# Optimization experiments

Measured on AMD Instinct MI355X. Metric: run time of the kernel, lower is better.

The kernel has to match this reference:

```python
import jax, jax.numpy as jnp
import numpy as np

EPS = 1e-10


def setup_inputs() -> dict:
    key = jax.random.key(0)
    k1, k2, k3 = jax.random.split(key, 3)
    B, N, S = 2, 16384, 4096
    return {
        "xyz": jax.random.normal(k1, (B, 3, N), dtype=jnp.float32),
        "sparse_xyz": jax.random.normal(k2, (B, 3, S), dtype=jnp.float32),
        "sparse_flow": jax.random.normal(k3, (B, 3, S), dtype=jnp.float32),
    }


def reference(xyz, sparse_xyz, sparse_flow):
    # channel-last views: x [B,N,3], s [B,S,3], f [B,S,3]
    x = jnp.transpose(xyz, (0, 2, 1))
    s = jnp.transpose(sparse_xyz, (0, 2, 1))
    f = jnp.transpose(sparse_flow, (0, 2, 1))

    # squared pairwise distances [B,N,S] (knn_point / square_distance)
    d2 = (
        jnp.sum(x * x, axis=-1)[:, :, None]
        + jnp.sum(s * s, axis=-1)[:, None, :]
        - 2.0 * jnp.einsum("bnc,bsc->bns", x, s)
    )
    # 3 nearest sparse neighbors of each dense point
    _, knn_idx = jax.lax.top_k(-d2, 3)  # [B,N,3]

    # index_points_group: gather neighbor coords/flows per batch
    gather = jax.vmap(lambda tbl, idx: tbl[idx])  # ([S,3],[N,3]) -> [N,3,3]
    grouped_xyz = gather(s, knn_idx)              # [B,N,3,3]
    grouped_flow = gather(f, knn_idx)             # [B,N,3,3]

    # inverse-distance weights (Euclidean dist, clamped)
    diff = grouped_xyz - x[:, :, None, :]
    dist = jnp.maximum(jnp.linalg.norm(diff, axis=3), EPS)  # [B,N,3]
    inv = 1.0 / dist
    weight = inv / jnp.sum(inv, axis=2, keepdims=True)      # [B,N,3]

    dense_flow = jnp.sum(weight[..., None] * grouped_flow, axis=2)  # [B,N,3]
    return jnp.transpose(dense_flow, (0, 2, 1))  # [B,3,N]
```

## Files before the change

### kernel.cpp

```cpp
#include <hip/hip_runtime.h>


constexpr int S_SPARSE = 4096;
constexpr int NSPLIT   = 64;
constexpr int Q        = 8;
constexpr int THREADS  = 256;
constexpr int PPB      = THREADS * Q / NSPLIT;
constexpr int NITER    = S_SPARSE / NSPLIT;
constexpr int K        = 3;
constexpr int KA       = 5;
constexpr int KM       = 8;
constexpr int KROW     = NSPLIT * K + 8;
constexpr int KBUF2_OFF_DW = PPB * KROW;
constexpr int SLIN_PAD = 64;

__device__ __forceinline__ unsigned med3u(unsigned a, unsigned b, unsigned c) {
    unsigned d;
    asm("v_med3_u32 %0, %1, %2, %3" : "=v"(d) : "v"(a), "v"(b), "v"(c));
    return d;
}

__global__ __launch_bounds__(THREADS)
void upsample_knn3(const float* __restrict__ xyz,
                   const float* __restrict__ sxyz,
                   const float* __restrict__ sflow,
                   float* __restrict__ out,
                   int N)
{
    __shared__ __align__(16) unsigned char smem_raw[(3 * S_SPARSE + SLIN_PAD) * 4];
    float*    slin = reinterpret_cast<float*>(smem_raw);
    unsigned* kbuf = reinterpret_cast<unsigned*>(smem_raw);

    const int b = blockIdx.y;
    const int t = threadIdx.x;
    const int g = t >> 6;
    const int s = t & 63;

    const float* sx = sxyz + (size_t)b * 3 * S_SPARSE;
    const float* sy = sx + S_SPARSE;
    const float* sz = sy + S_SPARSE;
    #pragma unroll
    for (int it = 0; it < 3 * S_SPARSE / (THREADS * 4); ++it) {
        const int j0 = (t + it * THREADS) * 4;
        *reinterpret_cast<float4*>(slin + j0) =
            *reinterpret_cast<const float4*>(sx + j0);
    }

    const float* xb = xyz + (size_t)b * 3 * N;
    const int p0 = blockIdx.x * PPB + g * Q;
    float qx[Q], qy[Q], qz[Q];
    {
        const float4 x0 = *reinterpret_cast<const float4*>(xb + p0);
        const float4 x1 = *reinterpret_cast<const float4*>(xb + p0 + 4);
        const float4 y0 = *reinterpret_cast<const float4*>(xb + N + p0);
        const float4 y1 = *reinterpret_cast<const float4*>(xb + N + p0 + 4);
        const float4 z0 = *reinterpret_cast<const float4*>(xb + 2 * N + p0);
        const float4 z1 = *reinterpret_cast<const float4*>(xb + 2 * N + p0 + 4);
        qx[0]=x0.x; qx[1]=x0.y; qx[2]=x0.z; qx[3]=x0.w; qx[4]=x1.x; qx[5]=x1.y; qx[6]=x1.z; qx[7]=x1.w;
        qy[0]=y0.x; qy[1]=y0.y; qy[2]=y0.z; qy[3]=y0.w; qy[4]=y1.x; qy[5]=y1.y; qy[6]=y1.z; qy[7]=y1.w;
        qz[0]=z0.x; qz[1]=z0.y; qz[2]=z0.z; qz[3]=z0.w; qz[4]=z1.x; qz[5]=z1.y; qz[6]=z1.z; qz[7]=z1.w;
    }
    __syncthreads();

    unsigned k0[Q], k1[Q], k2[Q];
    #pragma unroll
    for (int q = 0; q < Q; ++q) { k0[q]=0xFFFFFFFFu; k1[q]=0xFFFFFFFFu; k2[q]=0xFFFFFFFFu; }

    float px = slin[s], py = slin[s + S_SPARSE], pz = slin[s + 2 * S_SPARSE];

    #pragma unroll 4
    for (int i = 0; i < NITER; ++i) {
        const float cx = px, cy = py, cz = pz;
        const int   cj = (i << 6) | s;
        const int   jn = cj + 64;
        px = slin[jn];
        py = slin[jn + S_SPARSE];
        pz = slin[jn + 2 * S_SPARSE];
        #pragma unroll
        for (int q = 0; q < Q; ++q) {
            const float dx = qx[q] - cx;
            const float dy = qy[q] - cy;
            const float dz = qz[q] - cz;
            const float d2 = dx * dx + dy * dy + dz * dz;
            const unsigned c = (__float_as_uint(d2) & 0xFFFFF000u) | (unsigned)cj;
            k2[q] = med3u(k1[q], k2[q], c);
            k1[q] = med3u(k0[q], k1[q], c);
            k0[q] = min(k0[q], c);
        }
    }

    __syncthreads();
    #pragma unroll
    for (int q = 0; q < Q; ++q) {
        const int base = (g * Q + q) * KROW + s * K;
        kbuf[base + 0] = k0[q];
        kbuf[base + 1] = k1[q];
        kbuf[base + 2] = k2[q];
    }
    __syncthreads();

    {
        const int lp = t >> 3;
        const int ch = t & 7;
        unsigned m0=0xFFFFFFFFu, m1=0xFFFFFFFFu, m2=0xFFFFFFFFu, m3=0xFFFFFFFFu, m4=0xFFFFFFFFu;
        const unsigned* rowp = kbuf + lp * KROW + ch * 24;
        #pragma unroll
        for (int c = 0; c < 24; ++c) {
            const unsigned cc = rowp[c];
            m4 = med3u(m3, m4, cc);
            m3 = med3u(m2, m3, cc);
            m2 = med3u(m1, m2, cc);
            m1 = med3u(m0, m1, cc);
            m0 = min(m0, cc);
        }
        unsigned* o = kbuf + KBUF2_OFF_DW + (lp * 8 + ch) * KA;
        o[0]=m0; o[1]=m1; o[2]=m2; o[3]=m3; o[4]=m4;
    }
    __syncthreads();

    if (t < PPB) {
        unsigned bk[KM];
        #pragma unroll
        for (int k = 0; k < KM; ++k) bk[k] = 0xFFFFFFFFu;
        const unsigned* inp = kbuf + KBUF2_OFF_DW + t * 8 * KA;
        #pragma unroll
        for (int c = 0; c < 8 * KA; ++c) {
            const unsigned cc = inp[c];
            bk[7] = med3u(bk[6], bk[7], cc);
            bk[6] = med3u(bk[5], bk[6], cc);
            bk[5] = med3u(bk[4], bk[5], cc);
            bk[4] = med3u(bk[3], bk[4], cc);
            bk[3] = med3u(bk[2], bk[3], cc);
            bk[2] = med3u(bk[1], bk[2], cc);
            bk[1] = med3u(bk[0], bk[1], cc);
            bk[0] = min(bk[0], cc);
        }

        const int pt = blockIdx.x * PPB + t;
        const double qxd = (double)xb[pt];
        const double qyd = (double)xb[N + pt];
        const double qzd = (double)xb[2 * N + pt];

        double e0 = 1e300, e1 = 1e300, e2 = 1e300;
        int    j0 = 0,     j1 = 0,     j2 = 0;
        #pragma unroll
        for (int c = 0; c < KM; ++c) {
            const int    j  = (int)(bk[c] & 0xFFFu);
            const double dx = qxd - (double)sx[j];
            const double dy = qyd - (double)sy[j];
            const double dz = qzd - (double)sz[j];
            const double d2 = dx * dx + dy * dy + dz * dz;
            if (d2 < e2) {
                if (d2 < e1) {
                    e2 = e1; j2 = j1;
                    if (d2 < e0) { e1 = e0; j1 = j0; e0 = d2; j0 = j; }
                    else         { e1 = d2; j1 = j; }
                } else {
                    e2 = d2; j2 = j;
                }
            }
        }

        double dist0 = sqrt(e0); dist0 = dist0 > 1e-10 ? dist0 : 1e-10;
        double dist1 = sqrt(e1); dist1 = dist1 > 1e-10 ? dist1 : 1e-10;
        double dist2 = sqrt(e2); dist2 = dist2 > 1e-10 ? dist2 : 1e-10;
        const double inv0 = 1.0 / dist0;
        const double inv1 = 1.0 / dist1;
        const double inv2 = 1.0 / dist2;
        const double wsum = inv0 + inv1 + inv2;

        const float* fb = sflow + (size_t)b * 3 * S_SPARSE;
        float*       ob = out   + (size_t)b * 3 * N;
        #pragma unroll
        for (int c = 0; c < 3; ++c) {
            const float* fc = fb + c * S_SPARSE;
            const double o =
                (inv0 * (double)fc[j0] +
                 inv1 * (double)fc[j1] +
                 inv2 * (double)fc[j2]) / wsum;
            ob[c * N + pt] = (float)o;
        }
    }
}

extern "C" void kernel_launch(void* const* d_in, const int* in_sizes, int n_in,
                              void* d_out, int out_size, void* d_ws, size_t ws_size,
                              hipStream_t stream)
{
    const float* xyz  = (const float*)d_in[0];
    const float* sxyz = (const float*)d_in[1];
    const float* sflw = (const float*)d_in[2];
    float*       out  = (float*)d_out;

    const int B = 2;
    const int N = in_sizes[0] / (3 * B);

    dim3 grid(N / PPB, B);
    upsample_knn3<<<grid, THREADS, 0, stream>>>(xyz, sxyz, sflw, out, N);
}
```

Baseline: 44.22 us.

## Use expanded dot-product distance with packed float4 sparse points and 512-thread blocks

Sparse points are repacked in shared memory as float4 (x,y,z,|p|^2), so the inner loop issues one LDS per candidate and computes distance as three FMAs plus an add. A small positive offset keeps the value non-negative so the unsigned-key trick still works. The block grows to 512 threads and 64 points with a min-blocks hint, changing occupancy. The expanded form loses precision through cancellation, but the double-precision rescoring of the top-8 candidates should absorb this.

```diff
diff --git a/kernel.cpp b/kernel.cpp
--- a/kernel.cpp
+++ b/kernel.cpp
@@ -4,15 +4,15 @@
 constexpr int S_SPARSE = 4096;
 constexpr int NSPLIT   = 64;
 constexpr int Q        = 8;
-constexpr int THREADS  = 256;
-constexpr int PPB      = THREADS * Q / NSPLIT;
+constexpr int THREADS  = 512;
+constexpr int PPB      = 64;
 constexpr int NITER    = S_SPARSE / NSPLIT;
 constexpr int K        = 3;
 constexpr int KA       = 5;
 constexpr int KM       = 8;
 constexpr int KROW     = NSPLIT * K + 8;
 constexpr int KBUF2_OFF_DW = PPB * KROW;
-constexpr int SLIN_PAD = 64;
+constexpr int PQ_PAD   = 64;
 
 __device__ __forceinline__ unsigned med3u(unsigned a, unsigned b, unsigned c) {
     unsigned d;
@@ -20,35 +20,43 @@
     return d;
 }
 
-__global__ __launch_bounds__(THREADS)
+__global__ __launch_bounds__(THREADS, 4)
 void upsample_knn3(const float* __restrict__ xyz,
                    const float* __restrict__ sxyz,
                    const float* __restrict__ sflow,
                    float* __restrict__ out,
                    int N)
 {
-    __shared__ __align__(16) unsigned char smem_raw[(3 * S_SPARSE + SLIN_PAD) * 4];
-    float*    slin = reinterpret_cast<float*>(smem_raw);
+    __shared__ __align__(16) unsigned char smem_raw[(S_SPARSE + PQ_PAD) * 16];
+    float4*   pq   = reinterpret_cast<float4*>(smem_raw);
     unsigned* kbuf = reinterpret_cast<unsigned*>(smem_raw);
 
-    const int b = blockIdx.y;
-    const int t = threadIdx.x;
-    const int g = t >> 6;
-    const int s = t & 63;
+    const int t   = threadIdx.x;
+    const int s   = t & 63;
+    const int g   = t >> 6;
+    const int b   = blockIdx.y;
+    const int chk = blockIdx.x;
 
     const float* sx = sxyz + (size_t)b * 3 * S_SPARSE;
     const float* sy = sx + S_SPARSE;
     const float* sz = sy + S_SPARSE;
     #pragma unroll
-    for (int it = 0; it < 3 * S_SPARSE / (THREADS * 4); ++it) {
+    for (int it = 0; it < S_SPARSE / (THREADS * 4); ++it) {
         const int j0 = (t + it * THREADS) * 4;
-        *reinterpret_cast<float4*>(slin + j0) =
-            *reinterpret_cast<const float4*>(sx + j0);
+        const float4 vx = *reinterpret_cast<const float4*>(sx + j0);
+        const float4 vy = *reinterpret_cast<const float4*>(sy + j0);
+        const float4 vz = *reinterpret_cast<const float4*>(sz + j0);
+        #pragma unroll
+        for (int e = 0; e < 4; ++e) {
+            const float px = (&vx.x)[e], py = (&vy.x)[e], pz = (&vz.x)[e];
+            const float pp = fmaf(pz, pz, fmaf(py, py, px * px));
+            pq[j0 + e] = make_float4(px, py, pz, pp);
+        }
     }
 
     const float* xb = xyz + (size_t)b * 3 * N;
-    const int p0 = blockIdx.x * PPB + g * Q;
-    float qx[Q], qy[Q], qz[Q];
+    const int p0 = chk * PPB + g * Q;
+    float m2x[Q], m2y[Q], m2z[Q], qqc[Q];
     {
         const float4 x0 = *reinterpret_cast<const float4*>(xb + p0);
         const float4 x1 = *reinterpret_cast<const float4*>(xb + p0 + 4);
@@ -56,9 +64,16 @@
         const float4 y1 = *reinterpret_cast<const float4*>(xb + N + p0 + 4);
         const float4 z0 = *reinterpret_cast<const float4*>(xb + 2 * N + p0);
         const float4 z1 = *reinterpret_cast<const float4*>(xb + 2 * N + p0 + 4);
-        qx[0]=x0.x; qx[1]=x0.y; qx[2]=x0.z; qx[3]=x0.w; qx[4]=x1.x; qx[5]=x1.y; qx[6]=x1.z; qx[7]=x1.w;
-        qy[0]=y0.x; qy[1]=y0.y; qy[2]=y0.z; qy[3]=y0.w; qy[4]=y1.x; qy[5]=y1.y; qy[6]=y1.z; qy[7]=y1.w;
-        qz[0]=z0.x; qz[1]=z0.y; qz[2]=z0.z; qz[3]=z0.w; qz[4]=z1.x; qz[5]=z1.y; qz[6]=z1.z; qz[7]=z1.w;
+        #pragma unroll
+        for (int q = 0; q < Q; ++q) {
+            const float qx = (q < 4) ? (&x0.x)[q] : (&x1.x)[q - 4];
+            const float qy = (q < 4) ? (&y0.x)[q] : (&y1.x)[q - 4];
+            const float qz = (q < 4) ? (&z0.x)[q] : (&z1.x)[q - 4];
+            m2x[q] = -2.0f * qx;
+            m2y[q] = -2.0f * qy;
+            m2z[q] = -2.0f * qz;
+            qqc[q] = fmaf(qz, qz, fmaf(qy, qy, qx * qx)) + 1e-3f;
+        }
     }
     __syncthreads();
 
@@ -66,27 +81,23 @@
     #pragma unroll
     for (int q = 0; q < Q; ++q) { k0[q]=0xFFFFFFFFu; k1[q]=0xFFFFFFFFu; k2[q]=0xFFFFFFFFu; }
 
-    float px = slin[s], py = slin[s + S_SPARSE], pz = slin[s + 2 * S_SPARSE];
-
-    #pragma unroll 4
+    float4 cur = pq[s];
+    #pragma unroll 2
     for (int i = 0; i < NITER; ++i) {
-        const float cx = px, cy = py, cz = pz;
-        const int   cj = (i << 6) | s;
-        const int   jn = cj + 64;
-        px = slin[jn];
-        py = slin[jn + S_SPARSE];
-        pz = slin[jn + 2 * S_SPARSE];
+        const int j = (i << 6) | s;
+        const float4 nxt = pq[j + 64];
         #pragma unroll
         for (int q = 0; q < Q; ++q) {
-            const float dx = qx[q] - cx;
-            const float dy = qy[q] - cy;
-            const float dz = qz[q] - cz;
-            const float d2 = dx * dx + dy * dy + dz * dz;
-            const unsigned c = (__float_as_uint(d2) & 0xFFFFF000u) | (unsigned)cj;
+            const float v  = fmaf(m2x[q], cur.x,
+                             fmaf(m2y[q], cur.y,
+                             fmaf(m2z[q], cur.z, qqc[q])));
+            const float v2 = v + cur.w;
+            const unsigned c = (__float_as_uint(v2) & 0xFFFFF000u) | (unsigned)j;
             k2[q] = med3u(k1[q], k2[q], c);
             k1[q] = med3u(k0[q], k1[q], c);
             k0[q] = min(k0[q], c);
         }
+        cur = nxt;
     }
 
     __syncthreads();
@@ -102,7 +113,8 @@
     {
         const int lp = t >> 3;
         const int ch = t & 7;
-        unsigned m0=0xFFFFFFFFu, m1=0xFFFFFFFFu, m2=0xFFFFFFFFu, m3=0xFFFFFFFFu, m4=0xFFFFFFFFu;
+        unsigned m0=0xFFFFFFFFu, m1=0xFFFFFFFFu, m2=0xFFFFFFFFu,
+                 m3=0xFFFFFFFFu, m4=0xFFFFFFFFu;
         const unsigned* rowp = kbuf + lp * KROW + ch * 24;
         #pragma unroll
         for (int c = 0; c < 24; ++c) {
@@ -136,7 +148,7 @@
             bk[0] = min(bk[0], cc);
         }
 
-        const int pt = blockIdx.x * PPB + t;
+        const int pt = chk * PPB + t;
         const double qxd = (double)xb[pt];
         const double qyd = (double)xb[N + pt];
         const double qzd = (double)xb[2 * N + pt];
```

Result: faster. 39.54 us, median of 2 (-10.6%).
